# Kernel optimization log

Measured on AMD Instinct MI355X. Metric: run time of the kernel, lower is better.

The kernel has to match this reference:

```python
import jax, jax.numpy as jnp
import numpy as np


def gcn_conv(x, W, b, src, dst, n_nodes):
    # PyG GCNConv: out = D^{-1/2} (A+I) D^{-1/2} X W + b  (self-loops already in src/dst)
    h = x @ W  # [N, F_out]
    ones = jnp.ones(src.shape[0], dtype=h.dtype)
    deg = jax.ops.segment_sum(ones, dst, num_segments=n_nodes)  # in-degree incl. self-loop
    dinv = jnp.where(deg > 0, jax.lax.rsqrt(deg), 0.0)
    norm = dinv[src] * dinv[dst]  # [E]
    msg = h[src] * norm[:, None]  # gather + scale, [E, F_out]
    out = jax.ops.segment_sum(msg, dst, num_segments=n_nodes)  # scatter-add
    return out + b


def setup_inputs() -> dict:
    key = jax.random.key(0)
    ks = jax.random.split(key, 5)
    N, E, F_in, H, F_out = 50000, 800000, 128, 128, 64
    x = jax.random.normal(ks[0], (N, F_in), dtype=jnp.float32)
    edge_index = jax.random.randint(ks[1], (2, E), 0, N, dtype=jnp.int64)
    W1 = jax.random.normal(ks[2], (F_in, H), dtype=jnp.float32) / np.sqrt(F_in)
    b1 = jnp.zeros((H,), dtype=jnp.float32)
    W3 = jax.random.normal(ks[3], (H, F_out), dtype=jnp.float32) / np.sqrt(H)
    b3 = jnp.zeros((F_out,), dtype=jnp.float32)
    W4 = jax.random.normal(ks[4], (H, F_out), dtype=jnp.float32) / np.sqrt(H)
    b4 = jnp.zeros((F_out,), dtype=jnp.float32)
    return {"x": x, "edge_index": edge_index, "W1": W1, "b1": b1,
            "W3": W3, "b3": b3, "W4": W4, "b4": b4}


def reference(x, edge_index, W1, b1, W3, b3, W4, b4):
    n_nodes = x.shape[0]
    loops = jnp.arange(n_nodes, dtype=edge_index.dtype)
    src = jnp.concatenate([edge_index[0], loops])
    dst = jnp.concatenate([edge_index[1], loops])
    h = jax.nn.relu(gcn_conv(x, W1, b1, src, dst, n_nodes))  # dropout p=0.0 is identity
    mean = gcn_conv(h, W3, b3, src, dst, n_nodes)
    std = gcn_conv(h, W4, b4, src, dst, n_nodes)
    return (mean, std)
```

## Files before the change

kernel.cpp:

```cpp
#include <hip/hip_runtime.h>

typedef unsigned int uint_t;
typedef unsigned short ushort_t;

constexpr int MAXDEG = 64;

static __device__ __forceinline__ uint_t f2bf_bits(float f) {
  uint_t u = __builtin_bit_cast(uint_t, f);
  return (u + 0x7fffu + ((u >> 16) & 1u)) >> 16;
}
static __device__ __forceinline__ uint_t pack_bf2(float lo, float hi) {
  return f2bf_bits(lo) | (f2bf_bits(hi) << 16);
}
static __device__ __forceinline__ float bf_lo(uint_t u) {
  return __builtin_bit_cast(float, u << 16);
}
static __device__ __forceinline__ float bf_hi(uint_t u) {
  return __builtin_bit_cast(float, u & 0xffff0000u);
}

typedef __attribute__((ext_vector_type(4))) float  v4f;
typedef __attribute__((ext_vector_type(2))) uint_t v2u;
typedef __attribute__((ext_vector_type(8))) short  short8_t;
typedef __attribute__((ext_vector_type(4))) float  f32x4_t;

static __device__ __forceinline__ int ldnt_i(const int* p) {
  return __builtin_nontemporal_load(p);
}
static __device__ __forceinline__ void stnt_u2(uint_t* p, uint_t a, uint_t b) {
  v2u t; t.x = a; t.y = b;
  __builtin_nontemporal_store(t, (v2u*)p);
}

static inline size_t align256(size_t x) { return (x + 255) & ~(size_t)255; }

static __device__ __forceinline__ void lds_fence_barrier() {
  asm volatile("s_waitcnt lgkmcnt(0)" ::: "memory");
  __builtin_amdgcn_s_barrier();
}

template<typename IdxT>
__global__ __launch_bounds__(256, 3) void gemm1_fill_kernel(
    const float* __restrict__ X, const float* __restrict__ W1,
    uint_t* __restrict__ outG, int Nrows,
    const int* __restrict__ src, const int* __restrict__ dst,
    int* __restrict__ cursor, IdxT* __restrict__ edge, int E) {
  __shared__ float wlds[64][128];
  __shared__ float xT[64][68];

  const int tid = threadIdx.x;
  const int gtid = blockIdx.x * 256 + tid;
  const int T = gridDim.x * 256;

  for (int e = gtid + 4 * T; e < E; e += T) {
    int d = dst[e], s = src[e];
    int slot = atomicAdd(&cursor[d], 1);
    if (slot < MAXDEG) edge[(size_t)d * MAXDEG + slot] = (IdxT)s;
  }

  int d[4], s[4];
#pragma unroll
  for (int k = 0; k < 4; ++k) {
    int e = gtid + k * T;
    bool ok = (e < E);
    int ee = ok ? e : 0;
    d[k] = ldnt_i(dst + ee);
    s[k] = ldnt_i(src + ee);
    if (!ok) d[k] = Nrows;
  }

  const int rowbase = blockIdx.x * 64;
  const int r = tid >> 2;
  const bool valid = (rowbase + r) < Nrows;
  float4 w0[8], w1t[8], x0[4], x1t[4];
  {
    int rg = rowbase + r;
    int rs = valid ? rg : (Nrows - 1);
    const float4* xrow = (const float4*)(X + (size_t)rs * 128);
#pragma unroll
    for (int i = 0; i < 8; ++i) {
      int f = tid + i * 256;
      int kk = f >> 5, cc = f & 31;
      w0[i]  = ((const float4*)W1)[(size_t)kk * 32 + cc];
      w1t[i] = ((const float4*)W1)[(size_t)(64 + kk) * 32 + cc];
    }
#pragma unroll
    for (int p = 0; p < 4; ++p) {
      int kf4 = (tid & 3) + p * 4;
      x0[p]  = xrow[kf4];
      x1t[p] = xrow[16 + kf4];
    }
  }
  __builtin_amdgcn_sched_barrier(0);

  int slot[4];
#pragma unroll
  for (int k = 0; k < 4; ++k) slot[k] = atomicAdd(&cursor[d[k]], 1);
  __builtin_amdgcn_sched_barrier(0);

  const int cg = tid & 31;
  const int rl = tid >> 5;

  float acc[8][4];
#pragma unroll
  for (int i = 0; i < 8; ++i)
#pragma unroll
    for (int j = 0; j < 4; ++j) acc[i][j] = 0.f;

#pragma unroll
  for (int i = 0; i < 8; ++i) {
    int f = tid + i * 256;
    int kk = f >> 5, cc = f & 31;
    *(float4*)&wlds[kk][cc * 4] = w0[i];
  }
#pragma unroll
  for (int p = 0; p < 4; ++p) {
    int kf4 = (tid & 3) + p * 4;
    float4 v = valid ? x0[p] : make_float4(0.f, 0.f, 0.f, 0.f);
    int ke = kf4 * 4;
    xT[ke + 0][r] = v.x;
    xT[ke + 1][r] = v.y;
    xT[ke + 2][r] = v.z;
    xT[ke + 3][r] = v.w;
  }
  lds_fence_barrier();

#pragma unroll 8
  for (int kk = 0; kk < 64; ++kk) {
    float4 xa = *(const float4*)&xT[kk][rl * 8];
    float4 xb = *(const float4*)&xT[kk][rl * 8 + 4];
    float4 wv = *(const float4*)&wlds[kk][cg * 4];
    float xr[8] = {xa.x, xa.y, xa.z, xa.w, xb.x, xb.y, xb.z, xb.w};
    float wc[4] = {wv.x, wv.y, wv.z, wv.w};
#pragma unroll
    for (int i = 0; i < 8; ++i)
#pragma unroll
      for (int j = 0; j < 4; ++j)
        acc[i][j] = fmaf(xr[i], wc[j], acc[i][j]);
  }
  lds_fence_barrier();

#pragma unroll
  for (int i = 0; i < 8; ++i) {
    int f = tid + i * 256;
    int kk = f >> 5, cc = f & 31;
    *(float4*)&wlds[kk][cc * 4] = w1t[i];
  }
#pragma unroll
  for (int p = 0; p < 4; ++p) {
    int kf4 = (tid & 3) + p * 4;
    float4 v = valid ? x1t[p] : make_float4(0.f, 0.f, 0.f, 0.f);
    int ke = kf4 * 4;
    xT[ke + 0][r] = v.x;
    xT[ke + 1][r] = v.y;
    xT[ke + 2][r] = v.z;
    xT[ke + 3][r] = v.w;
  }
  lds_fence_barrier();

#pragma unroll 8
  for (int kk = 0; kk < 64; ++kk) {
    float4 xa = *(const float4*)&xT[kk][rl * 8];
    float4 xb = *(const float4*)&xT[kk][rl * 8 + 4];
    float4 wv = *(const float4*)&wlds[kk][cg * 4];
    float xr[8] = {xa.x, xa.y, xa.z, xa.w, xb.x, xb.y, xb.z, xb.w};
    float wc[4] = {wv.x, wv.y, wv.z, wv.w};
#pragma unroll
    for (int i = 0; i < 8; ++i)
#pragma unroll
      for (int j = 0; j < 4; ++j)
        acc[i][j] = fmaf(xr[i], wc[j], acc[i][j]);
  }

#pragma unroll
  for (int i = 0; i < 8; ++i) {
    int rr = rowbase + rl * 8 + i;
    if (rr >= Nrows) continue;
    stnt_u2(outG + (size_t)rr * 64 + cg * 2,
            pack_bf2(acc[i][0], acc[i][1]), pack_bf2(acc[i][2], acc[i][3]));
  }
#pragma unroll
  for (int k = 0; k < 4; ++k) {
    if (slot[k] < MAXDEG) edge[(size_t)d[k] * MAXDEG + slot[k]] = (IdxT)s[k];
  }
}

__global__ __launch_bounds__(256) void pack_w_kernel(
    const float* __restrict__ W3, const float* __restrict__ W4,
    ushort_t* __restrict__ Bhi, ushort_t* __restrict__ Blo) {
  int u = blockIdx.x * 256 + threadIdx.x;
  int l = u & 63, kk = (u >> 6) & 3, t = u >> 8;
  int q = l >> 4, c = l & 15;
  int n = t * 16 + c;
  short8_t vh, vl;
#pragma unroll
  for (int j = 0; j < 8; ++j) {
    int k = kk * 32 + q * 8 + j;
    float w = (n < 64) ? W3[(size_t)k * 64 + n] : W4[(size_t)k * 64 + (n - 64)];
    uint_t hb = f2bf_bits(w);
    float wl = w - __builtin_bit_cast(float, hb << 16);
    vh[j] = (short)hb;
    vl[j] = (short)f2bf_bits(wl);
  }
  *(short8_t*)(Bhi + (size_t)u * 8) = vh;
  *(short8_t*)(Blo + (size_t)u * 8) = vl;
}

__global__ __launch_bounds__(256) void gemm2_mfma_kernel(
    const ushort_t* __restrict__ Xbf, const ushort_t* __restrict__ Bhi,
    const ushort_t* __restrict__ Blo, const float* __restrict__ b3,
    const float* __restrict__ b4, float* __restrict__ outM,
    float* __restrict__ outS, int Nrows) {
  const int tid = threadIdx.x;
  const int wid = tid >> 6;
  const int lane = tid & 63;
  const int q = lane >> 4;
  const int c = lane & 15;
  const int rowbase = blockIdx.x * 64 + wid * 16;

  f32x4_t acc[8];
#pragma unroll
  for (int t = 0; t < 8; ++t) acc[t] = (f32x4_t){0.f, 0.f, 0.f, 0.f};

  int arow = rowbase + c;
  int ars = (arow < Nrows) ? arow : (Nrows - 1);
  const ushort_t* abase = Xbf + (size_t)ars * 128 + q * 8;

#pragma unroll
  for (int kk = 0; kk < 4; ++kk) {
    short8_t a = __builtin_nontemporal_load((const short8_t*)(abase + kk * 32));
#pragma unroll
    for (int t = 0; t < 8; ++t) {
      const size_t fo = ((size_t)(t * 4 + kk) * 64 + lane) * 8;
      short8_t bh = *(const short8_t*)(Bhi + fo);
      short8_t bl = *(const short8_t*)(Blo + fo);
      acc[t] = __builtin_amdgcn_mfma_f32_16x16x32_bf16(a, bh, acc[t], 0, 0, 0);
      acc[t] = __builtin_amdgcn_mfma_f32_16x16x32_bf16(a, bl, acc[t], 0, 0, 0);
    }
  }

#pragma unroll
  for (int t = 0; t < 8; ++t) {
    float bias = (t < 4) ? b3[t * 16 + c] : b4[(t - 4) * 16 + c];
    float* obase = (t < 4) ? (outM + t * 16 + c) : (outS + (t - 4) * 16 + c);
#pragma unroll
    for (int rr = 0; rr < 4; ++rr) {
      int row = rowbase + q * 4 + rr;
      if (row < Nrows)
        __builtin_nontemporal_store(acc[t][rr] + bias, obase + (size_t)row * 64);
    }
  }
}

template<int EPI, bool SRCDV, typename IdxT>
__global__ __launch_bounds__(256) void aggregate_kernel(
    const uint_t* __restrict__ g, const int* __restrict__ deg,
    const IdxT* __restrict__ edge, const float* __restrict__ b1,
    uint_t* __restrict__ out, int Nn) {
  const int wave = threadIdx.x >> 6;
  const int lane = threadIdx.x & 63;
  const int n = blockIdx.x * 4 + wave;
  if (n >= Nn) return;
  const int dn = deg[n];
  const int cnt = (dn > 63) ? 63 : dn;
  const float sc = rsqrtf((float)(dn + 1));

  int vl = n;
  if (lane >= 1 && lane <= cnt) vl = (int)edge[(size_t)n * MAXDEG + (lane - 1)];
  float wl = 0.f;
  if (lane == 0)        wl = SRCDV ? sc : 1.f;
  else if (lane <= cnt) wl = SRCDV ? rsqrtf((float)(deg[vl] + 1)) : 1.f;

  const int h = lane >> 5;
  const int c = lane & 31;
  const uint_t* gc = g + c * 2;

  float a0 = 0.f, a1 = 0.f, a2 = 0.f, a3 = 0.f;
  const int entries = cnt + 1;
  const int npairs = (entries + 1) >> 1;

  int p = 0;
  for (; p + 4 <= npairs; p += 4) {
    int ss[4]; float ww[4]; uint2 uu[4];
#pragma unroll
    for (int t = 0; t < 4; ++t) {
      int j = 2 * (p + t) + h;
      ss[t] = __shfl(vl, j);
      ww[t] = __shfl(wl, j);
    }
#pragma unroll
    for (int t = 0; t < 4; ++t)
      uu[t] = *(const uint2*)(gc + (size_t)ss[t] * 64);
#pragma unroll
    for (int t = 0; t < 4; ++t) {
      a0 = fmaf(ww[t], bf_lo(uu[t].x), a0);
      a1 = fmaf(ww[t], bf_hi(uu[t].x), a1);
      a2 = fmaf(ww[t], bf_lo(uu[t].y), a2);
      a3 = fmaf(ww[t], bf_hi(uu[t].y), a3);
    }
  }
  for (; p < npairs; ++p) {
    int j = 2 * p + h;
    int s0 = __shfl(vl, j);
    float w0 = __shfl(wl, j);
    uint2 u = *(const uint2*)(gc + (size_t)s0 * 64);
    a0 = fmaf(w0, bf_lo(u.x), a0);
    a1 = fmaf(w0, bf_hi(u.x), a1);
    a2 = fmaf(w0, bf_lo(u.y), a2);
    a3 = fmaf(w0, bf_hi(u.y), a3);
  }

  a0 += __shfl_xor(a0, 32);
  a1 += __shfl_xor(a1, 32);
  a2 += __shfl_xor(a2, 32);
  a3 += __shfl_xor(a3, 32);

  if (h == 0) {
    if (EPI == 1) {
      float4 b = ((const float4*)b1)[c];
      a0 = fmaxf(fmaf(sc, a0, b.x), 0.f) * sc;
      a1 = fmaxf(fmaf(sc, a1, b.y), 0.f) * sc;
      a2 = fmaxf(fmaf(sc, a2, b.z), 0.f) * sc;
      a3 = fmaxf(fmaf(sc, a3, b.w), 0.f) * sc;
    } else {
      a0 *= sc; a1 *= sc; a2 *= sc; a3 *= sc;
    }
    stnt_u2(out + (size_t)n * 64 + c * 2, pack_bf2(a0, a1), pack_bf2(a2, a3));
  }
}

extern "C" void kernel_launch(void* const* d_in, const int* in_sizes, int n_in,
                              void* d_out, int out_size, void* d_ws, size_t ws_size,
                              hipStream_t stream) {
  const float* x  = (const float*)d_in[0];
  const int*   ei = (const int*)d_in[1];
  const float* W1 = (const float*)d_in[2];
  const float* b1 = (const float*)d_in[3];
  const float* W3 = (const float*)d_in[4];
  const float* b3 = (const float*)d_in[5];
  const float* W4 = (const float*)d_in[6];
  const float* b4 = (const float*)d_in[7];

  const int N = in_sizes[0] / 128;
  const int E = in_sizes[1] / 2;
  const int* src = ei;
  const int* dst = ei + E;

  char* w = (char*)d_ws;
  size_t off = 0;
  auto carve = [&](size_t bytes) { void* p = w + off; off = align256(off + bytes); return p; };
  int*      cursor = (int*)carve((size_t)(N + 1) * sizeof(int));
  void*     edge   = carve((size_t)(N + 1) * MAXDEG * sizeof(int));
  uint_t*   bufG   = (uint_t*)carve((size_t)N * 64 * sizeof(uint_t));
  uint_t*   bufH   = (uint_t*)carve((size_t)N * 64 * sizeof(uint_t));
  ushort_t* Bhi    = (ushort_t*)carve((size_t)16384 * sizeof(ushort_t));
  ushort_t* Blo    = (ushort_t*)carve((size_t)16384 * sizeof(ushort_t));

  float* out_mean = (float*)d_out;
  float* out_std  = out_mean + (size_t)N * 64;

  hipMemsetAsync(cursor, 0, (size_t)(N + 1) * sizeof(int), stream);

  const int gblocks = (N + 63) / 64;
  const int ablocks = (N + 3) / 4;

  pack_w_kernel<<<8, 256, 0, stream>>>(W3, W4, Bhi, Blo);

  if (N <= 65535) {
    ushort_t* es = (ushort_t*)edge;
    gemm1_fill_kernel<ushort_t><<<gblocks, 256, 0, stream>>>(
        x, W1, bufG, N, src, dst, cursor, es, E);
    aggregate_kernel<1, true,  ushort_t><<<ablocks, 256, 0, stream>>>(bufG, cursor, es, b1, bufH, N);
    aggregate_kernel<2, false, ushort_t><<<ablocks, 256, 0, stream>>>(bufH, cursor, es, nullptr, bufG, N);
  } else {
    int* es = (int*)edge;
    gemm1_fill_kernel<int><<<gblocks, 256, 0, stream>>>(
        x, W1, bufG, N, src, dst, cursor, es, E);
    aggregate_kernel<1, true,  int><<<ablocks, 256, 0, stream>>>(bufG, cursor, es, b1, bufH, N);
    aggregate_kernel<2, false, int><<<ablocks, 256, 0, stream>>>(bufH, cursor, es, nullptr, bufG, N);
  }
  gemm2_mfma_kernel<<<gblocks, 256, 0, stream>>>(
      (const ushort_t*)bufG, Bhi, Blo, b3, b4, out_mean, out_std, N);
}
```

Before: 156.6 us.

## Build per-node edge lists via two-pass bucket sort instead of global atomics

Replaces the global-atomic per-node edge fill that was fused into the first GEMM with a two-stage bucketing scheme. Edges are first scattered into up to 64 coarse destination buckets using a shared-memory histogram, then each bucket is expanded into per-node rows in LDS and written out with coalesced vector stores. The first GEMM becomes a standalone kernel with a simple K loop. This aims to remove scattered global atomics and random 2-byte writes, at the cost of extra kernel launches, a bucket staging buffer, and losing the overlap of edge filling with the GEMM.

```diff
diff --git a/kernel.cpp b/kernel.cpp
--- a/kernel.cpp
+++ b/kernel.cpp
@@ -19,14 +19,10 @@
   return __builtin_bit_cast(float, u & 0xffff0000u);
 }
 
-typedef __attribute__((ext_vector_type(4))) float  v4f;
 typedef __attribute__((ext_vector_type(2))) uint_t v2u;
 typedef __attribute__((ext_vector_type(8))) short  short8_t;
 typedef __attribute__((ext_vector_type(4))) float  f32x4_t;
 
-static __device__ __forceinline__ int ldnt_i(const int* p) {
-  return __builtin_nontemporal_load(p);
-}
 static __device__ __forceinline__ void stnt_u2(uint_t* p, uint_t a, uint_t b) {
   v2u t; t.x = a; t.y = b;
   __builtin_nontemporal_store(t, (v2u*)p);
@@ -34,154 +30,153 @@
 
 static inline size_t align256(size_t x) { return (x + 255) & ~(size_t)255; }
 
-static __device__ __forceinline__ void lds_fence_barrier() {
-  asm volatile("s_waitcnt lgkmcnt(0)" ::: "memory");
-  __builtin_amdgcn_s_barrier();
-}
-
-template<typename IdxT>
-__global__ __launch_bounds__(256, 3) void gemm1_fill_kernel(
+__global__ __launch_bounds__(256) void bucket_scatter_kernel(
+    const int* __restrict__ src, const int* __restrict__ dst,
+    uint2* __restrict__ buckets, int* __restrict__ bucketcnt,
+    int E, int C, int shift) {
+  __shared__ int hist[64];
+  __shared__ int base[64];
+  const int tid = threadIdx.x;
+  const int e0 = blockIdx.x * 2048;
+
+  if (tid < 64) hist[tid] = 0;
+  __syncthreads();
+
+  int dd[8], ss[8], slot[8];
+#pragma unroll
+  for (int i = 0; i < 8; ++i) {
+    int e = e0 + tid + i * 256;
+    bool ok = (e < E);
+    dd[i] = ok ? dst[e] : -1;
+    ss[i] = ok ? src[e] : 0;
+    slot[i] = ok ? atomicAdd(&hist[dd[i] >> shift], 1) : 0;
+  }
+  __syncthreads();
+
+  if (tid < 64) {
+    int c = hist[tid];
+    base[tid] = (c > 0) ? atomicAdd(&bucketcnt[tid], c) : 0;
+  }
+  __syncthreads();
+
+#pragma unroll
+  for (int i = 0; i < 8; ++i) {
+    if (dd[i] < 0) continue;
+    int b = dd[i] >> shift;
+    int pos = base[b] + slot[i];
+    if (pos < C)
+      buckets[(size_t)b * C + pos] = make_uint2((uint_t)dd[i], (uint_t)ss[i]);
+  }
+}
+
+template<typename IdxT, int WIN>
+__global__ __launch_bounds__(256) void bucket_to_rows_kernel(
+    const uint2* __restrict__ buckets, const int* __restrict__ bucketcnt,
+    IdxT* __restrict__ edge, int* __restrict__ deg, int Nn, int C, int shift) {
+  __shared__ __align__(16) IdxT rows[WIN * MAXDEG];
+  __shared__ int cnt[WIN];
+  const int tid = threadIdx.x;
+  const int b = blockIdx.x;
+  const int node0 = b << shift;
+  const int RANGE = 1 << shift;
+  int ec = bucketcnt[b];
+  if (ec > C) ec = C;
+  const uint2* bb = buckets + (size_t)b * C;
+
+  for (int w0 = 0; w0 < RANGE; w0 += WIN) {
+    for (int i = tid; i < WIN; i += 256) cnt[i] = 0;
+    __syncthreads();
+    for (int i = tid; i < ec; i += 256) {
+      uint2 it = bb[i];
+      int local = (int)it.x - node0 - w0;
+      if (local >= 0 && local < WIN) {
+        int sl = atomicAdd(&cnt[local], 1);
+        if (sl < MAXDEG) rows[local * MAXDEG + sl] = (IdxT)it.y;
+      }
+    }
+    __syncthreads();
+    const int nbase = node0 + w0;
+    constexpr int PER = (MAXDEG * sizeof(IdxT)) / 16;
+    const uint4* rv = (const uint4*)rows;
+    uint4* ev = (uint4*)(edge + (size_t)nbase * MAXDEG);
+    for (int i = tid; i < WIN * PER; i += 256) {
+      int node = nbase + i / PER;
+      if (node < Nn) ev[i] = rv[i];
+    }
+    for (int i = tid; i < WIN; i += 256) {
+      int node = nbase + i;
+      if (node < Nn) deg[node] = cnt[i];
+    }
+    __syncthreads();
+  }
+}
+
+__global__ __launch_bounds__(256) void gemm1_kernel(
     const float* __restrict__ X, const float* __restrict__ W1,
-    uint_t* __restrict__ outG, int Nrows,
-    const int* __restrict__ src, const int* __restrict__ dst,
-    int* __restrict__ cursor, IdxT* __restrict__ edge, int E) {
-  __shared__ float wlds[64][128];
-  __shared__ float xT[64][68];
+    uint_t* __restrict__ outG, int Nrows) {
+  constexpr int BK = 64;
+  __shared__ float wlds[BK][128];
+  __shared__ float xT[BK][68];
 
   const int tid = threadIdx.x;
-  const int gtid = blockIdx.x * 256 + tid;
-  const int T = gridDim.x * 256;
-
-  for (int e = gtid + 4 * T; e < E; e += T) {
-    int d = dst[e], s = src[e];
-    int slot = atomicAdd(&cursor[d], 1);
-    if (slot < MAXDEG) edge[(size_t)d * MAXDEG + slot] = (IdxT)s;
-  }
-
-  int d[4], s[4];
-#pragma unroll
-  for (int k = 0; k < 4; ++k) {
-    int e = gtid + k * T;
-    bool ok = (e < E);
-    int ee = ok ? e : 0;
-    d[k] = ldnt_i(dst + ee);
-    s[k] = ldnt_i(src + ee);
-    if (!ok) d[k] = Nrows;
-  }
-
+  const int cg = tid & 31;
+  const int rl = tid >> 5;
   const int rowbase = blockIdx.x * 64;
-  const int r = tid >> 2;
-  const bool valid = (rowbase + r) < Nrows;
-  float4 w0[8], w1t[8], x0[4], x1t[4];
-  {
-    int rg = rowbase + r;
-    int rs = valid ? rg : (Nrows - 1);
-    const float4* xrow = (const float4*)(X + (size_t)rs * 128);
+
+  float acc[8][4];
+#pragma unroll
+  for (int i = 0; i < 8; ++i)
+#pragma unroll
+    for (int j = 0; j < 4; ++j) acc[i][j] = 0.f;
+
+  for (int k0 = 0; k0 < 128; k0 += BK) {
+    __syncthreads();
 #pragma unroll
     for (int i = 0; i < 8; ++i) {
       int f = tid + i * 256;
       int kk = f >> 5, cc = f & 31;
-      w0[i]  = ((const float4*)W1)[(size_t)kk * 32 + cc];
-      w1t[i] = ((const float4*)W1)[(size_t)(64 + kk) * 32 + cc];
-    }
-#pragma unroll
-    for (int p = 0; p < 4; ++p) {
-      int kf4 = (tid & 3) + p * 4;
-      x0[p]  = xrow[kf4];
-      x1t[p] = xrow[16 + kf4];
-    }
-  }
-  __builtin_amdgcn_sched_barrier(0);
-
-  int slot[4];
-#pragma unroll
-  for (int k = 0; k < 4; ++k) slot[k] = atomicAdd(&cursor[d[k]], 1);
-  __builtin_amdgcn_sched_barrier(0);
-
-  const int cg = tid & 31;
-  const int rl = tid >> 5;
-
-  float acc[8][4];
-#pragma unroll
-  for (int i = 0; i < 8; ++i)
-#pragma unroll
-    for (int j = 0; j < 4; ++j) acc[i][j] = 0.f;
-
+      float4 v = ((const float4*)W1)[(size_t)(k0 + kk) * 32 + cc];
+      *(float4*)&wlds[kk][cc * 4] = v;
+    }
+    {
+      int r = tid >> 2;
+      int rg = rowbase + r;
+      int rs = (rg < Nrows) ? rg : (Nrows - 1);
+      const float4* xrow = (const float4*)(X + (size_t)rs * 128);
+      bool valid = (rg < Nrows);
+#pragma unroll
+      for (int p = 0; p < 4; ++p) {
+        int kf4 = (tid & 3) + p * 4;
+        float4 v = xrow[(k0 >> 2) + kf4];
+        if (!valid) v = make_float4(0.f, 0.f, 0.f, 0.f);
+        int ke = kf4 * 4;
+        xT[ke + 0][r] = v.x;
+        xT[ke + 1][r] = v.y;
+        xT[ke + 2][r] = v.z;
+        xT[ke + 3][r] = v.w;
+      }
+    }
+    __syncthreads();
+#pragma unroll 8
+    for (int kk = 0; kk < BK; ++kk) {
+      float4 xa = *(const float4*)&xT[kk][rl * 8];
+      float4 xb = *(const float4*)&xT[kk][rl * 8 + 4];
+      float4 wv = *(const float4*)&wlds[kk][cg * 4];
+      float xr[8] = {xa.x, xa.y, xa.z, xa.w, xb.x, xb.y, xb.z, xb.w};
+      float wc[4] = {wv.x, wv.y, wv.z, wv.w};
+#pragma unroll
+      for (int i = 0; i < 8; ++i)
+#pragma unroll
+        for (int j = 0; j < 4; ++j)
+          acc[i][j] = fmaf(xr[i], wc[j], acc[i][j]);
+    }
+  }
 #pragma unroll
   for (int i = 0; i < 8; ++i) {
-    int f = tid + i * 256;
-    int kk = f >> 5, cc = f & 31;
-    *(float4*)&wlds[kk][cc * 4] = w0[i];
-  }
-#pragma unroll
-  for (int p = 0; p < 4; ++p) {
-    int kf4 = (tid & 3) + p * 4;
-    float4 v = valid ? x0[p] : make_float4(0.f, 0.f, 0.f, 0.f);
-    int ke = kf4 * 4;
-    xT[ke + 0][r] = v.x;
-    xT[ke + 1][r] = v.y;
-    xT[ke + 2][r] = v.z;
-    xT[ke + 3][r] = v.w;
-  }
-  lds_fence_barrier();
-
-#pragma unroll 8
-  for (int kk = 0; kk < 64; ++kk) {
-    float4 xa = *(const float4*)&xT[kk][rl * 8];
-    float4 xb = *(const float4*)&xT[kk][rl * 8 + 4];
-    float4 wv = *(const float4*)&wlds[kk][cg * 4];
-    float xr[8] = {xa.x, xa.y, xa.z, xa.w, xb.x, xb.y, xb.z, xb.w};
-    float wc[4] = {wv.x, wv.y, wv.z, wv.w};
-#pragma unroll
-    for (int i = 0; i < 8; ++i)
-#pragma unroll
-      for (int j = 0; j < 4; ++j)
-        acc[i][j] = fmaf(xr[i], wc[j], acc[i][j]);
-  }
-  lds_fence_barrier();
-
-#pragma unroll
-  for (int i = 0; i < 8; ++i) {
-    int f = tid + i * 256;
-    int kk = f >> 5, cc = f & 31;
-    *(float4*)&wlds[kk][cc * 4] = w1t[i];
-  }
-#pragma unroll
-  for (int p = 0; p < 4; ++p) {
-    int kf4 = (tid & 3) + p * 4;
-    float4 v = valid ? x1t[p] : make_float4(0.f, 0.f, 0.f, 0.f);
-    int ke = kf4 * 4;
-    xT[ke + 0][r] = v.x;
-    xT[ke + 1][r] = v.y;
-    xT[ke + 2][r] = v.z;
-    xT[ke + 3][r] = v.w;
-  }
-  lds_fence_barrier();
-
-#pragma unroll 8
-  for (int kk = 0; kk < 64; ++kk) {
-    float4 xa = *(const float4*)&xT[kk][rl * 8];
-    float4 xb = *(const float4*)&xT[kk][rl * 8 + 4];
-    float4 wv = *(const float4*)&wlds[kk][cg * 4];
-    float xr[8] = {xa.x, xa.y, xa.z, xa.w, xb.x, xb.y, xb.z, xb.w};
-    float wc[4] = {wv.x, wv.y, wv.z, wv.w};
-#pragma unroll
-    for (int i = 0; i < 8; ++i)
-#pragma unroll
-      for (int j = 0; j < 4; ++j)
-        acc[i][j] = fmaf(xr[i], wc[j], acc[i][j]);
-  }
-
-#pragma unroll
-  for (int i = 0; i < 8; ++i) {
-    int rr = rowbase + rl * 8 + i;
-    if (rr >= Nrows) continue;
-    stnt_u2(outG + (size_t)rr * 64 + cg * 2,
+    int r = rowbase + rl * 8 + i;
+    if (r >= Nrows) continue;
+    stnt_u2(outG + (size_t)r * 64 + cg * 2,
             pack_bf2(acc[i][0], acc[i][1]), pack_bf2(acc[i][2], acc[i][3]));
-  }
-#pragma unroll
-  for (int k = 0; k < 4; ++k) {
-    if (slot[k] < MAXDEG) edge[(size_t)d[k] * MAXDEG + slot[k]] = (IdxT)s[k];
   }
 }
 
@@ -345,39 +340,52 @@
   const int E = in_sizes[1] / 2;
   const int* src = ei;
   const int* dst = ei + E;
+  const bool small = (N <= 65535);
+  const size_t esz = small ? sizeof(ushort_t) : sizeof(int);
+
+  int shift = 10;
+  while (((N + (1 << shift) - 1) >> shift) > 64) ++shift;
+  const int NB = (N + (1 << shift) - 1) >> shift;
+  const int C = (E / NB) * 3 / 2 + 1024;
 
   char* w = (char*)d_ws;
   size_t off = 0;
   auto carve = [&](size_t bytes) { void* p = w + off; off = align256(off + bytes); return p; };
-  int*      cursor = (int*)carve((size_t)(N + 1) * sizeof(int));
-  void*     edge   = carve((size_t)(N + 1) * MAXDEG * sizeof(int));
-  uint_t*   bufG   = (uint_t*)carve((size_t)N * 64 * sizeof(uint_t));
-  uint_t*   bufH   = (uint_t*)carve((size_t)N * 64 * sizeof(uint_t));
-  ushort_t* Bhi    = (ushort_t*)carve((size_t)16384 * sizeof(ushort_t));
-  ushort_t* Blo    = (ushort_t*)carve((size_t)16384 * sizeof(ushort_t));
+  int*      deg       = (int*)carve((size_t)N * sizeof(int));
+  int*      bucketcnt = (int*)carve(64 * sizeof(int));
+  uint2*    buckets   = (uint2*)carve((size_t)NB * C * sizeof(uint2));
+  void*     edge      = carve((size_t)N * MAXDEG * esz);
+  uint_t*   bufG      = (uint_t*)carve((size_t)N * 64 * sizeof(uint_t));
+  uint_t*   bufH      = (uint_t*)carve((size_t)N * 64 * sizeof(uint_t));
+  ushort_t* Bhi       = (ushort_t*)carve((size_t)16384 * sizeof(ushort_t));
+  ushort_t* Blo       = (ushort_t*)carve((size_t)16384 * sizeof(ushort_t));
 
   float* out_mean = (float*)d_out;
   float* out_std  = out_mean + (size_t)N * 64;
 
-  hipMemsetAsync(cursor, 0, (size_t)(N + 1) * sizeof(int), stream);
+  hipMemsetAsync(bucketcnt, 0, 64 * sizeof(int), stream);
 
   const int gblocks = (N + 63) / 64;
   const int ablocks = (N + 3) / 4;
+  const int sblocks = (E + 2047) / 2048;
 
   pack_w_kernel<<<8, 256, 0, stream>>>(W3, W4, Bhi, Blo);
-
-  if (N <= 65535) {
+  bucket_scatter_kernel<<<sblocks, 256, 0, stream>>>(src, dst, buckets, bucketcnt, E, C, shift);
+
+  if (small) {
     ushort_t* es = (ushort_t*)edge;
-    gemm1_fill_kernel<ushort_t><<<gblocks, 256, 0, stream>>>(
-        x, W1, bufG, N, src, dst, cursor, es, E);
-    aggregate_kernel<1, true,  ushort_t><<<ablocks, 256, 0, stream>>>(bufG, cursor, es, b1, bufH, N);
-    aggregate_kernel<2, false, ushort_t><<<ablocks, 256, 0, stream>>>(bufH, cursor, es, nullptr, bufG, N);
+    bucket_to_rows_kernel<ushort_t, 1024><<<NB, 256, 0, stream>>>(
+        buckets, bucketcnt, es, deg, N, C, shift);
+    gemm1_kernel<<<gblocks, 256, 0, stream>>>(x, W1, bufG, N);
+    aggregate_kernel<1, true,  ushort_t><<<ablocks, 256, 0, stream>>>(bufG, deg, es, b1, bufH, N);
+    aggregate_kernel<2, false, ushort_t><<<ablocks, 256, 0, stream>>>(bufH, deg, es, nullptr, bufG, N);
   } else {
     int* es = (int*)edge;
-    gemm1_fill_kernel<int><<<gblocks, 256, 0, stream>>>(
-        x, W1, bufG, N, src, dst, cursor, es, E);
-    aggregate_kernel<1, true,  int><<<ablocks, 256, 0, stream>>>(bufG, cursor, es, b1, bufH, N);
-    aggregate_kernel<2, false, int><<<ablocks, 256, 0, stream>>>(bufH, cursor, es, nullptr, bufG, N);
+    bucket_to_rows_kernel<int, 512><<<NB, 256, 0, stream>>>(
+        buckets, bucketcnt, es, deg, N, C, shift);
+    gemm1_kernel<<<gblocks, 256, 0, stream>>>(x, W1, bufG, N);
+    aggregate_kernel<1, true,  int><<<ablocks, 256, 0, stream>>>(bufG, deg, es, b1, bufH, N);
+    aggregate_kernel<2, false, int><<<ablocks, 256, 0, stream>>>(bufH, deg, es, nullptr, bufG, N);
   }
   gemm2_mfma_kernel<<<gblocks, 256, 0, stream>>>(
       (const ushort_t*)bufG, Bhi, Blo, b3, b4, out_mean, out_std, N);
```

After: 177.6 us. +13.4%, slower.
